# Performance work log

Measured on AMD Instinct MI355X. Metric: run time of the kernel, lower is better.

Reference implementation:

```python
import jax, jax.numpy as jnp
import numpy as np

G, T, S, M = 2048, 256, 32, 8


def setup_inputs() -> dict:
    key = jax.random.key(0)
    k_in, k_F, k_H, k_Q, k_R = jax.random.split(key, 5)
    inp = jax.random.normal(k_in, (G, T, M), dtype=jnp.float32)
    I_s = jnp.eye(S, dtype=jnp.float32)
    # Stable transition matrix: near-identity with small random perturbation
    F = 0.95 * I_s + 0.05 * jax.random.normal(k_F, (S, S), dtype=jnp.float32) / jnp.sqrt(S * 1.0)
    H = jax.random.normal(k_H, (M, S), dtype=jnp.float32) / jnp.sqrt(S * 1.0)
    Lq = jax.random.normal(k_Q, (S, S), dtype=jnp.float32) / jnp.sqrt(S * 1.0)
    Q = 0.01 * (Lq @ Lq.T) + 1e-4 * I_s  # process noise (PSD)
    Lr = jax.random.normal(k_R, (M, M), dtype=jnp.float32) / jnp.sqrt(M * 1.0)
    R = 0.1 * (Lr @ Lr.T) + 1e-3 * jnp.eye(M, dtype=jnp.float32)  # measurement noise (PSD)
    m0 = jnp.zeros((G, S), dtype=jnp.float32)
    P0 = jnp.broadcast_to(I_s, (G, S, S)).astype(jnp.float32)
    return {"input": inp, "F": F, "H": H, "Q": Q, "R": R, "m0": m0, "P0": P0}


def _kalman_filter(inp, F, H, Q, R, m0, P0):
    """One-step-ahead measurement predictions, matching KalmanFilter.forward:
    at each t emit measurement of the prior, then update with obs[t] and predict."""

    def step(carry, obs_t):
        m, P = carry  # m: [G,S], P: [G,S,S] (prior at time t)
        # --- compute_measurement(H, R) on the prior ---
        meas_mean = m @ H.T                                   # [G,M]
        HP = jnp.einsum('ms,gsk->gmk', H, P)                  # [G,M,S]
        S_t = jnp.einsum('gmk,nk->gmn', HP, H) + R            # [G,M,M]
        # --- update(obs_t) ---
        resid = obs_t - meas_mean                             # [G,M]
        KT = jnp.linalg.solve(S_t, HP)                        # [G,M,S] = S^{-1} H P = K^T
        m_upd = m + jnp.einsum('gms,gm->gs', KT, resid)       # [G,S]
        P_upd = P - jnp.einsum('gmi,gmk->gik', KT, HP)        # (I-KH)P
        P_upd = 0.5 * (P_upd + jnp.swapaxes(P_upd, -1, -2))   # symmetrize (numerics)
        # --- predict(F, Q) ---
        m_next = m_upd @ F.T
        P_next = jnp.einsum('ij,gjk,lk->gil', F, P_upd, F) + Q
        return (m_next, P_next), (meas_mean, S_t)

    obs_T = jnp.swapaxes(inp, 0, 1)                           # [T,G,M]
    _, (means, covs) = jax.lax.scan(step, (m0, P0), obs_T)
    return jnp.swapaxes(means, 0, 1), jnp.swapaxes(covs, 0, 1)  # [G,T,M], [G,T,M,M]


def reference(input, F, H, Q, R, m0, P0):
    return _kalman_filter(input, F, H, Q, R, m0, P0)
```

## Files before the change

kernel.cpp:

```cpp
#include <hip/hip_runtime.h>

#define G_N 2048
#define T_N 256
#define S_N 32
#define M_N 8

#define A_OFF 0
#define B_OFF 262144
#define S_OFF (262144 + 65536)

#define OUT_TOTAL 37748736ull
#define EL 3072
#define SCRATCH_FLOATS (EL + 2ull * 256 * EL)

__global__ __launch_bounds__(1024) void kf_init(
    const float* __restrict__ F, const float* __restrict__ H,
    const float* __restrict__ Q, const float* __restrict__ R,
    float* __restrict__ base)
{
    __shared__ float Hs[8][33], Rl[8][9], Rinv[8][9], RH[8][33];
    const int tid = threadIdx.x;
    if (tid < 256) Hs[tid >> 5][tid & 31] = H[tid];
    if (tid < 64)  Rl[tid >> 3][tid & 7] = R[tid];
    __syncthreads();
    if (tid < 64) {
        int r = tid >> 3, c = tid & 7;
        float a = Rl[r][c];
        float b = (r == c) ? 1.f : 0.f;
#pragma unroll
        for (int j = 0; j < 8; ++j) {
            float ajj  = __shfl(a, j * 8 + j, 64);
            float pinv = 1.0f / ajj;
            if (r == j) { a *= pinv; b *= pinv; }
            float ajc = __shfl(a, j * 8 + c, 64);
            float bjc = __shfl(b, j * 8 + c, 64);
            float arj = __shfl(a, r * 8 + j, 64);
            if (r != j) { a -= arj * ajc; b -= arj * bjc; }
        }
        Rinv[r][c] = b;
    }
    __syncthreads();
    if (tid < 256) {
        int m = tid >> 5, j = tid & 31;
        float s = 0.f;
#pragma unroll
        for (int n = 0; n < 8; ++n) s += Rinv[m][n] * Hs[n][j];
        RH[m][j] = s;
    }
    __syncthreads();
    {
        int i = tid >> 5, j = tid & 31;
        float g = 0.f;
#pragma unroll
        for (int m = 0; m < 8; ++m) g += Hs[m][i] * RH[m][j];
        base[2048 + tid] = g;
    }
    base[tid] = Q[tid];
    base[1024 + tid] = F[tid];
}

__global__ __launch_bounds__(1024) void kf_level(
    const float* __restrict__ in, float* __restrict__ out,
    const float* __restrict__ base, int dist)
{
    const int bi = blockIdx.x;
    const int tid = threadIdx.x;
    const int r = tid >> 5, c = tid & 31;
    float* o = out + (size_t)bi * EL;

    if (bi < dist) {
        const float* s = base ? base : in + (size_t)bi * EL;
        o[tid] = s[tid]; o[tid + 1024] = s[tid + 1024]; o[tid + 2048] = s[tid + 2048];
        return;
    }
    const float* pa = base ? base : in + (size_t)(bi - dist) * EL;
    const float* pb = base ? base : in + (size_t)bi * EL;

    __shared__ float Ea[32][33], Fa[32][33], Ga[32][33];
    __shared__ float Eb[32][33], Fb[32][33], Gb[32][33];
    __shared__ float T1[32][33], T3[32][33], T4[32][33], T5[32][33], T6[32][33];
    __shared__ float Kf[32][33], Msv[32][33];
    __shared__ float Aug[32][67];

    Ea[r][c] = pa[tid]; Fa[r][c] = pa[tid + 1024]; Ga[r][c] = pa[tid + 2048];
    Eb[r][c] = pb[tid]; Fb[r][c] = pb[tid + 1024]; Gb[r][c] = pb[tid + 2048];
    __syncthreads();

    {
        float acc = (r == c) ? 1.f : 0.f;
#pragma unroll
        for (int k = 0; k < 32; ++k) acc += Gb[r][k] * Ea[k][c];
        Aug[r][c] = acc; Msv[r][c] = acc;
        Aug[r][32 + c] = (r == c) ? 1.f : 0.f;
    }
    __syncthreads();

    for (int jb = 0; jb < 16; ++jb) {
        const int p0 = 2 * jb, p1 = p0 + 1;
        float a00 = Aug[p0][p0], a01 = Aug[p0][p1], a10 = Aug[p1][p0], a11 = Aug[p1][p1];
        float m0 = Aug[r][p0], m1 = Aug[r][p1];
        float q0 = Aug[p0][c], q1 = Aug[p1][c];
        float q0b = Aug[p0][32 + c], q1b = Aug[p1][32 + c];
        float x0 = Aug[r][c], x1 = Aug[r][32 + c];
        __syncthreads();
        float id = 1.0f / (a00 * a11 - a01 * a10);
        float i00 = a11 * id, i01 = -a01 * id, i10 = -a10 * id, i11 = a00 * id;
        float n0, n1;
        if (r == p0)      { n0 = i00 * q0 + i01 * q1;  n1 = i00 * q0b + i01 * q1b; }
        else if (r == p1) { n0 = i10 * q0 + i11 * q1;  n1 = i10 * q0b + i11 * q1b; }
        else {
            float L0 = m0 * i00 + m1 * i10, L1 = m0 * i01 + m1 * i11;
            n0 = x0 - L0 * q0 - L1 * q1;
            n1 = x1 - L0 * q0b - L1 * q1b;
        }
        Aug[r][c] = n0; Aug[r][32 + c] = n1;
        __syncthreads();
    }

    {
        float acc = 0.f;
#pragma unroll
        for (int k = 0; k < 32; ++k) acc += Msv[r][k] * Aug[k][32 + c];
        T6[r][c] = acc;
    }
    __syncthreads();
    {
        float acc = 0.f;
#pragma unroll
        for (int k = 0; k < 32; ++k) acc += Aug[r][32 + k] * T6[k][c];
        Kf[r][c] = 2.0f * Aug[r][32 + c] - acc;
    }
    __syncthreads();

    {
        float a1 = 0.f, a3 = 0.f, a4 = 0.f;
#pragma unroll
        for (int k = 0; k < 32; ++k) {
            a1 += Ea[r][k] * Kf[k][c];
            a3 += Fb[r][k] * Kf[c][k];
            a4 += Kf[r][k] * Gb[k][c];
        }
        T1[r][c] = a1; T3[r][c] = a3; T4[r][c] = a4;
    }
    __syncthreads();
    {
        float b1 = 0.f, b2 = 0.f;
#pragma unroll
        for (int k = 0; k < 32; ++k) {
            b1 += Fb[r][k] * T1[k][c];
            b2 += T3[r][k] * Fa[k][c];
        }
        T6[r][c] = b1; T5[r][c] = b2;
    }
    __syncthreads();
    {
        float c1 = Eb[r][c], c2 = 0.f;
#pragma unroll
        for (int k = 0; k < 32; ++k) {
            c1 += T6[r][k] * Fb[c][k];
            c2 += Fa[k][r] * T4[k][c];
        }
        Msv[r][c] = c1; T1[r][c] = c2;
    }
    __syncthreads();
    {
        float d1 = Ga[r][c];
#pragma unroll
        for (int k = 0; k < 32; ++k) d1 += T1[r][k] * Fa[k][c];
        T3[r][c] = d1;
    }
    __syncthreads();
    o[tid]        = 0.5f * (Msv[r][c] + Msv[c][r]);
    o[1024 + tid] = T5[r][c];
    o[2048 + tid] = 0.5f * (T3[r][c] + T3[c][r]);
}

__global__ __launch_bounds__(1024) void kf_final(
    const float* __restrict__ elems, const float* __restrict__ F,
    const float* __restrict__ H, const float* __restrict__ R,
    const float* __restrict__ P0, float* __restrict__ ws)
{
    const int t = blockIdx.x;
    const int tid = threadIdx.x;
    const int r = tid >> 5, c = tid & 31;

    __shared__ float Pm[32][33], Fs[32][33], P0s[32][33];
    __shared__ float Et[32][33], Ft[32][33], Gt[32][33], Yv[32][33], Tt[32][33];
    __shared__ float Hs[8][33], HP[8][33], Wm[8][33], Um[8][33];
    __shared__ float Ss[8][9], Rs[8][9], Si[8][9];
    __shared__ float Aug[32][67];

    Fs[r][c] = F[tid];
    if (tid < 256) Hs[tid >> 5][tid & 31] = H[tid];
    if (tid < 64)  Rs[tid >> 3][tid & 7] = R[tid];
    P0s[r][c] = P0[tid];
    __syncthreads();

    if (t == 0) {
        Pm[r][c] = P0s[r][c];
        __syncthreads();
    } else {
        const float* el = elems + (size_t)(t - 1) * EL;
        Et[r][c] = el[tid]; Ft[r][c] = el[tid + 1024]; Gt[r][c] = el[tid + 2048];
        __syncthreads();
        {
            float acc = (r == c) ? 1.f : 0.f;
#pragma unroll
            for (int k = 0; k < 32; ++k) acc += Gt[r][k] * P0s[k][c];
            Aug[r][c] = acc;
            Aug[r][32 + c] = (r == c) ? 1.f : 0.f;
        }
        __syncthreads();
        for (int jb = 0; jb < 16; ++jb) {
            const int p0 = 2 * jb, p1 = p0 + 1;
            float a00 = Aug[p0][p0], a01 = Aug[p0][p1], a10 = Aug[p1][p0], a11 = Aug[p1][p1];
            float m0 = Aug[r][p0], m1 = Aug[r][p1];
            float q0 = Aug[p0][c], q1 = Aug[p1][c];
            float q0b = Aug[p0][32 + c], q1b = Aug[p1][32 + c];
            float x0 = Aug[r][c], x1 = Aug[r][32 + c];
            __syncthreads();
            float id = 1.0f / (a00 * a11 - a01 * a10);
            float i00 = a11 * id, i01 = -a01 * id, i10 = -a10 * id, i11 = a00 * id;
            float n0, n1;
            if (r == p0)      { n0 = i00 * q0 + i01 * q1;  n1 = i00 * q0b + i01 * q1b; }
            else if (r == p1) { n0 = i10 * q0 + i11 * q1;  n1 = i10 * q0b + i11 * q1b; }
            else {
                float L0 = m0 * i00 + m1 * i10, L1 = m0 * i01 + m1 * i11;
                n0 = x0 - L0 * q0 - L1 * q1;
                n1 = x1 - L0 * q0b - L1 * q1b;
            }
            Aug[r][c] = n0; Aug[r][32 + c] = n1;
            __syncthreads();
        }
        {
            float acc = 0.f;
#pragma unroll
            for (int k = 0; k < 32; ++k) acc += P0s[r][k] * Aug[k][32 + c];
            Yv[r][c] = acc;
        }
        __syncthreads();
        {
            float acc = 0.f;
#pragma unroll
            for (int k = 0; k < 32; ++k) acc += Ft[r][k] * Yv[k][c];
            Tt[r][c] = acc;
        }
        __syncthreads();
        {
            float acc = Et[r][c];
#pragma unroll
            for (int k = 0; k < 32; ++k) acc += Tt[r][k] * Ft[c][k];
            Pm[r][c] = acc;
        }
        __syncthreads();
        {
            float ps = 0.5f * (Pm[r][c] + Pm[c][r]);
            __syncthreads();
            Pm[r][c] = ps;
            __syncthreads();
        }
    }

    float* A_tab = ws + A_OFF;
    float* B_tab = ws + B_OFF;
    float* S_tab = ws + S_OFF;

    if (tid < 256) {
        int m = tid >> 5, k = tid & 31;
        float acc = 0.f;
#pragma unroll
        for (int j = 0; j < 32; ++j) acc += Hs[m][j] * Pm[j][k];
        HP[m][k] = acc;
    }
    __syncthreads();
    if (tid < 64) {
        int m = tid >> 3, n = tid & 7;
        float sv = Rs[m][n];
#pragma unroll
        for (int k = 0; k < 32; ++k) sv += HP[m][k] * Hs[n][k];
        Ss[m][n] = sv;
        S_tab[t * 64 + m * 8 + n] = sv;
    }
    if (tid >= 256 && tid < 512) {
        int e = tid - 256, m = e >> 5, j = e & 31;
        float wv = 0.f;
#pragma unroll
        for (int k = 0; k < 32; ++k) wv += HP[m][k] * Fs[j][k];
        Wm[m][j] = wv;
    }
    __syncthreads();
    if (tid < 64) {
        int rr = tid >> 3, cc = tid & 7;
        float a = Ss[rr][cc];
        float b = (rr == cc) ? 1.f : 0.f;
#pragma unroll
        for (int j = 0; j < 8; ++j) {
            float ajj  = __shfl(a, j * 8 + j, 64);
            float pinv = 1.0f / ajj;
            if (rr == j) { a *= pinv; b *= pinv; }
            float ajc = __shfl(a, j * 8 + cc, 64);
            float bjc = __shfl(b, j * 8 + cc, 64);
            float arj = __shfl(a, rr * 8 + j, 64);
            if (rr != j) { a -= arj * ajc; b -= arj * bjc; }
        }
        Si[rr][cc] = b;
    }
    __syncthreads();
    if (tid < 256) {
        int m = tid >> 5, s = tid & 31;
        float u = 0.f;
#pragma unroll
        for (int n = 0; n < 8; ++n) u += Si[m][n] * Wm[n][s];
        Um[m][s] = u;
        B_tab[t * 256 + s * 8 + m] = u;
    }
    __syncthreads();
    {
        float a = Fs[r][c];
#pragma unroll
        for (int m = 0; m < 8; ++m) a -= Um[m][r] * Hs[m][c];
        A_tab[t * 1024 + tid] = a;
    }
}

__global__ __launch_bounds__(256) void kf_means(
    const float* __restrict__ obs, const float* __restrict__ H,
    const float* __restrict__ m0, const float* __restrict__ ws,
    float* __restrict__ out)
{
    __shared__ float As[S_N][36];
    __shared__ float Bs[S_N][12];
    __shared__ float4 Sls[16];

    const int tid = threadIdx.x;
    const int gl = tid >> 5, s = tid & 31;
    const int g = blockIdx.x * 8 + gl;

    const float4* A4 = (const float4*)(ws + A_OFF);
    const float4* B4 = (const float4*)(ws + B_OFF);
    const float4* S4 = (const float4*)(ws + S_OFF);
    float* means = out;
    float4* covs4 = (float4*)(out + (size_t)G_N * T_N * M_N);

    float Hreg[32];
#pragma unroll
    for (int k = 0; k < 32; ++k) Hreg[k] = (s < 8) ? H[s * 32 + k] : 0.f;

    float m_reg = m0[blockIdx.x * 256 + tid];

    float4 a4p = A4[tid];
    float4 b4p = (tid < 64) ? B4[tid] : make_float4(0, 0, 0, 0);
    float4 s4p = (tid < 16) ? S4[tid] : make_float4(0, 0, 0, 0);
    float u_reg = (s < 8) ? obs[((size_t)g * T_N + 0) * M_N + s] : 0.f;

    for (int t = 0; t < T_N; ++t) {
        {
            int rr = tid >> 3, c4w = tid & 7;
            *(float4*)&As[rr][4 * (((2 * rr) ^ c4w) & 7)] = a4p;
        }
        if (tid < 64) *(float4*)&Bs[tid >> 1][4 * (tid & 1)] = b4p;
        if (tid < 16) Sls[tid] = s4p;
        __syncthreads();

        if (t + 1 < T_N) {
            a4p = A4[(t + 1) * 256 + tid];
            if (tid < 64) b4p = B4[(t + 1) * 64 + tid];
            if (tid < 16) s4p = S4[(t + 1) * 16 + tid];
        }
        float u_next = 0.f;
        if (t + 1 < T_N && s < 8) u_next = obs[((size_t)g * T_N + (t + 1)) * M_N + s];

        if (tid < 128) {
            int gl2 = tid >> 4, cc = tid & 15;
            covs4[((size_t)(blockIdx.x * 8 + gl2) * T_N + t) * 16 + cc] = Sls[cc];
        }

        float acc = 0.f, accH = 0.f;
#pragma unroll
        for (int c4 = 0; c4 < 8; ++c4) {
            float4 a = *(const float4*)&As[s][4 * (((2 * s) ^ c4) & 7)];
            float mk0 = __shfl(m_reg, 4 * c4 + 0, 32);
            float mk1 = __shfl(m_reg, 4 * c4 + 1, 32);
            float mk2 = __shfl(m_reg, 4 * c4 + 2, 32);
            float mk3 = __shfl(m_reg, 4 * c4 + 3, 32);
            acc  += a.x * mk0 + a.y * mk1 + a.z * mk2 + a.w * mk3;
            accH += Hreg[4 * c4 + 0] * mk0 + Hreg[4 * c4 + 1] * mk1
                  + Hreg[4 * c4 + 2] * mk2 + Hreg[4 * c4 + 3] * mk3;
        }
#pragma unroll
        for (int mm = 0; mm < 8; ++mm) acc += Bs[s][mm] * __shfl(u_reg, mm, 32);

        if (s < 8) means[((size_t)g * T_N + t) * M_N + s] = accH;
        m_reg = acc;
        u_reg = u_next;
        __syncthreads();
    }
}

extern "C" void kernel_launch(void* const* d_in, const int* in_sizes, int n_in,
                              void* d_out, int out_size, void* d_ws, size_t ws_size,
                              hipStream_t stream) {
    const float* obs = (const float*)d_in[0];
    const float* F   = (const float*)d_in[1];
    const float* H   = (const float*)d_in[2];
    const float* Q   = (const float*)d_in[3];
    const float* R   = (const float*)d_in[4];
    const float* m0  = (const float*)d_in[5];
    const float* P0  = (const float*)d_in[6];
    float* out = (float*)d_out;
    float* ws  = (float*)d_ws;

    float* scratch = out + (OUT_TOTAL - SCRATCH_FLOATS);
    float* base = scratch;
    float* bufA = scratch + EL;
    float* bufB = bufA + 256ull * EL;

    kf_init<<<1, 1024, 0, stream>>>(F, H, Q, R, base);
    kf_level<<<256, 1024, 0, stream>>>(nullptr, bufA, base, 1);
    kf_level<<<256, 1024, 0, stream>>>(bufA, bufB, nullptr, 2);
    kf_level<<<256, 1024, 0, stream>>>(bufB, bufA, nullptr, 4);
    kf_level<<<256, 1024, 0, stream>>>(bufA, bufB, nullptr, 8);
    kf_level<<<256, 1024, 0, stream>>>(bufB, bufA, nullptr, 16);
    kf_level<<<256, 1024, 0, stream>>>(bufA, bufB, nullptr, 32);
    kf_level<<<256, 1024, 0, stream>>>(bufB, bufA, nullptr, 64);
    kf_level<<<256, 1024, 0, stream>>>(bufA, bufB, nullptr, 128);
    kf_final<<<256, 1024, 0, stream>>>(bufB, F, H, R, P0, ws);
    kf_means<<<G_N / 8, 256, 0, stream>>>(obs, H, m0, ws, out);
}
```

Measured before the change: 435.3 us.

## Replace prefix-scan levels with power-of-two compositions and chunked mean recurrence

The eight-level parallel prefix scan over covariance elements is replaced by a single-block computation of power-of-two compositions. A 31-block kernel then builds the composites, and each time step needs at most one extra composition. The sequential mean recurrence is split into 16 time chunks run in parallel with zero start state, then corrected by propagating chunk-end states through precomputed transition products and H-projected tables. This is meant to cut the launch count and serial depth, and to spread the mean work across more blocks. In exchange it adds scratch traffic in the output buffer and a separate cleanup pass for the tail covariance writes.

```diff
diff --git a/kernel.cpp b/kernel.cpp
--- a/kernel.cpp
+++ b/kernel.cpp
@@ -2,99 +2,45 @@
 
 #define G_N 2048
 #define T_N 256
-#define S_N 32
-#define M_N 8
 
 #define A_OFF 0
 #define B_OFF 262144
-#define S_OFF (262144 + 65536)
-
-#define OUT_TOTAL 37748736ull
-#define EL 3072
-#define SCRATCH_FLOATS (EL + 2ull * 256 * EL)
-
-__global__ __launch_bounds__(1024) void kf_init(
-    const float* __restrict__ F, const float* __restrict__ H,
-    const float* __restrict__ Q, const float* __restrict__ R,
-    float* __restrict__ base)
-{
-    __shared__ float Hs[8][33], Rl[8][9], Rinv[8][9], RH[8][33];
-    const int tid = threadIdx.x;
-    if (tid < 256) Hs[tid >> 5][tid & 31] = H[tid];
-    if (tid < 64)  Rl[tid >> 3][tid & 7] = R[tid];
-    __syncthreads();
+#define S_OFF 327680
+
+#define OUT_TOTAL  37748736ull
+#define EL         3072
+#define MEND_OFF   36498432ull
+#define HT_OFF     37547008ull
+#define PHI_OFF    37612544ull
+#define PW2_OFF    37628928ull
+#define PHP_OFF    37644288ull
+#define XT_OFF     37653504ull
+#define YT_OFF     37702656ull
+#define COVS4_BASE 1048576ull
+#define TAIL4_SKIP 8076032ull
+
+__device__ __forceinline__ void inv8_wave(int tid, float (*A8)[9], float (*O8)[9]) {
     if (tid < 64) {
         int r = tid >> 3, c = tid & 7;
-        float a = Rl[r][c];
+        float a = A8[r][c];
         float b = (r == c) ? 1.f : 0.f;
 #pragma unroll
         for (int j = 0; j < 8; ++j) {
-            float ajj  = __shfl(a, j * 8 + j, 64);
-            float pinv = 1.0f / ajj;
-            if (r == j) { a *= pinv; b *= pinv; }
+            float ajj = __shfl(a, j * 8 + j, 64);
+            float pv = 1.0f / ajj;
+            if (r == j) { a *= pv; b *= pv; }
             float ajc = __shfl(a, j * 8 + c, 64);
             float bjc = __shfl(b, j * 8 + c, 64);
             float arj = __shfl(a, r * 8 + j, 64);
             if (r != j) { a -= arj * ajc; b -= arj * bjc; }
         }
-        Rinv[r][c] = b;
-    }
-    __syncthreads();
-    if (tid < 256) {
-        int m = tid >> 5, j = tid & 31;
-        float s = 0.f;
-#pragma unroll
-        for (int n = 0; n < 8; ++n) s += Rinv[m][n] * Hs[n][j];
-        RH[m][j] = s;
-    }
-    __syncthreads();
-    {
-        int i = tid >> 5, j = tid & 31;
-        float g = 0.f;
-#pragma unroll
-        for (int m = 0; m < 8; ++m) g += Hs[m][i] * RH[m][j];
-        base[2048 + tid] = g;
-    }
-    base[tid] = Q[tid];
-    base[1024 + tid] = F[tid];
-}
-
-__global__ __launch_bounds__(1024) void kf_level(
-    const float* __restrict__ in, float* __restrict__ out,
-    const float* __restrict__ base, int dist)
-{
-    const int bi = blockIdx.x;
-    const int tid = threadIdx.x;
+        O8[r][c] = b;
+    }
+}
+
+__device__ __forceinline__ void inv32(int tid, float (*Aug)[66],
+                                      float (*Msv)[33], float (*Tmp)[33]) {
     const int r = tid >> 5, c = tid & 31;
-    float* o = out + (size_t)bi * EL;
-
-    if (bi < dist) {
-        const float* s = base ? base : in + (size_t)bi * EL;
-        o[tid] = s[tid]; o[tid + 1024] = s[tid + 1024]; o[tid + 2048] = s[tid + 2048];
-        return;
-    }
-    const float* pa = base ? base : in + (size_t)(bi - dist) * EL;
-    const float* pb = base ? base : in + (size_t)bi * EL;
-
-    __shared__ float Ea[32][33], Fa[32][33], Ga[32][33];
-    __shared__ float Eb[32][33], Fb[32][33], Gb[32][33];
-    __shared__ float T1[32][33], T3[32][33], T4[32][33], T5[32][33], T6[32][33];
-    __shared__ float Kf[32][33], Msv[32][33];
-    __shared__ float Aug[32][67];
-
-    Ea[r][c] = pa[tid]; Fa[r][c] = pa[tid + 1024]; Ga[r][c] = pa[tid + 2048];
-    Eb[r][c] = pb[tid]; Fb[r][c] = pb[tid + 1024]; Gb[r][c] = pb[tid + 2048];
-    __syncthreads();
-
-    {
-        float acc = (r == c) ? 1.f : 0.f;
-#pragma unroll
-        for (int k = 0; k < 32; ++k) acc += Gb[r][k] * Ea[k][c];
-        Aug[r][c] = acc; Msv[r][c] = acc;
-        Aug[r][32 + c] = (r == c) ? 1.f : 0.f;
-    }
-    __syncthreads();
-
     for (int jb = 0; jb < 16; ++jb) {
         const int p0 = 2 * jb, p1 = p0 + 1;
         float a00 = Aug[p0][p0], a01 = Aug[p0][p1], a10 = Aug[p1][p0], a11 = Aug[p1][p1];
@@ -116,161 +62,225 @@
         Aug[r][c] = n0; Aug[r][32 + c] = n1;
         __syncthreads();
     }
-
+    float acc = 0.f;
+#pragma unroll
+    for (int k = 0; k < 32; ++k) acc += Msv[r][k] * Aug[k][32 + c];
+    Tmp[r][c] = acc;
+    __syncthreads();
+    acc = 0.f;
+#pragma unroll
+    for (int k = 0; k < 32; ++k) acc += Aug[r][32 + k] * Tmp[k][c];
+    float kv = 2.0f * Aug[r][32 + c] - acc;
+    __syncthreads();
+    Aug[r][c] = kv;
+    __syncthreads();
+}
+
+__device__ __forceinline__ void compose(int tid,
+    float (*Ea)[33], float (*Fa)[33], float (*Ga)[33],
+    float (*Eb)[33], float (*Fb)[33], float (*Gb)[33],
+    float (*Msv)[33], float (*T1)[33], float (*T3)[33],
+    float (*T4)[33], float (*T5)[33], float (*Aug)[66]) {
+    const int r = tid >> 5, c = tid & 31;
+    float acc = (r == c) ? 1.f : 0.f;
+#pragma unroll
+    for (int k = 0; k < 32; ++k) acc += Gb[r][k] * Ea[k][c];
+    Aug[r][c] = acc; Msv[r][c] = acc; Aug[r][32 + c] = (r == c) ? 1.f : 0.f;
+    __syncthreads();
+    inv32(tid, Aug, Msv, T4);
+    float a1 = 0, a3 = 0, a4 = 0;
+#pragma unroll
+    for (int k = 0; k < 32; ++k) {
+        a1 += Ea[r][k] * Aug[k][c];
+        a3 += Fb[r][k] * Aug[c][k];
+        a4 += Aug[r][k] * Gb[k][c];
+    }
+    T1[r][c] = a1; T3[r][c] = a3; T4[r][c] = a4;
+    __syncthreads();
+    float b1 = 0, b2 = 0;
+#pragma unroll
+    for (int k = 0; k < 32; ++k) {
+        b1 += Fb[r][k] * T1[k][c];
+        b2 += T3[r][k] * Fa[k][c];
+    }
+    Aug[r][32 + c] = b1; T5[r][c] = b2;
+    __syncthreads();
+    float c1 = Eb[r][c], c2 = 0;
+#pragma unroll
+    for (int k = 0; k < 32; ++k) {
+        c1 += Aug[r][32 + k] * Fb[c][k];
+        c2 += Fa[k][r] * T4[k][c];
+    }
+    __syncthreads();
+    Msv[r][c] = c1; T1[r][c] = c2;
+    __syncthreads();
+    float d1 = Ga[r][c];
+#pragma unroll
+    for (int k = 0; k < 32; ++k) d1 += T1[r][k] * Fa[k][c];
+    __syncthreads();
+    T3[r][c] = d1;
+    __syncthreads();
+}
+
+__device__ __forceinline__ void load_el(const float* g, int tid,
+    float (*E)[33], float (*F)[33], float (*G)[33]) {
+    const int r = tid >> 5, c = tid & 31;
+    E[r][c] = g[tid]; F[r][c] = g[tid + 1024]; G[r][c] = g[tid + 2048];
+}
+__device__ __forceinline__ void store_el(float* g, int tid,
+    float (*E)[33], float (*F)[33], float (*G)[33]) {
+    const int r = tid >> 5, c = tid & 31;
+    g[tid] = E[r][c]; g[tid + 1024] = F[r][c]; g[tid + 2048] = G[r][c];
+}
+__device__ __forceinline__ void copy_res_sym(int tid,
+    float (*Msv)[33], float (*T5)[33], float (*T3)[33],
+    float (*E)[33], float (*F)[33], float (*G)[33]) {
+    const int r = tid >> 5, c = tid & 31;
+    float e = 0.5f * (Msv[r][c] + Msv[c][r]);
+    float f = T5[r][c];
+    float gg = 0.5f * (T3[r][c] + T3[c][r]);
+    E[r][c] = e; F[r][c] = f; G[r][c] = gg;
+    __syncthreads();
+}
+
+#define COMPOSE_SHARED \
+    __shared__ float Ea[32][33], Fa[32][33], Ga[32][33]; \
+    __shared__ float Eb[32][33], Fb[32][33], Gb[32][33]; \
+    __shared__ float Msv[32][33], T1[32][33], T3[32][33], T4[32][33], T5[32][33]; \
+    __shared__ float Aug[32][66];
+
+__global__ __launch_bounds__(1024) void kf_pow1(
+    const float* __restrict__ F, const float* __restrict__ H,
+    const float* __restrict__ Q, const float* __restrict__ R,
+    float* __restrict__ out)
+{
+    COMPOSE_SHARED
+    __shared__ float Rl[8][9], Ri[8][9];
+    const int tid = threadIdx.x, r = tid >> 5, c = tid & 31;
+
+    Ea[r][c] = Q[tid];
+    Fa[r][c] = F[tid];
+    if (tid < 256) T1[tid >> 5][tid & 31] = H[tid];
+    if (tid < 64)  Rl[tid >> 3][tid & 7] = R[tid];
+    __syncthreads();
+    inv8_wave(tid, Rl, Ri);
+    __syncthreads();
+    if (tid < 256) {
+        int m = tid >> 5, j = tid & 31;
+        float s = 0.f;
+#pragma unroll
+        for (int n = 0; n < 8; ++n) s += Ri[m][n] * T1[n][j];
+        T3[m][j] = s;
+    }
+    __syncthreads();
     {
-        float acc = 0.f;
-#pragma unroll
-        for (int k = 0; k < 32; ++k) acc += Msv[r][k] * Aug[k][32 + c];
-        T6[r][c] = acc;
-    }
-    __syncthreads();
-    {
-        float acc = 0.f;
-#pragma unroll
-        for (int k = 0; k < 32; ++k) acc += Aug[r][32 + k] * T6[k][c];
-        Kf[r][c] = 2.0f * Aug[r][32 + c] - acc;
-    }
-    __syncthreads();
-
-    {
-        float a1 = 0.f, a3 = 0.f, a4 = 0.f;
-#pragma unroll
-        for (int k = 0; k < 32; ++k) {
-            a1 += Ea[r][k] * Kf[k][c];
-            a3 += Fb[r][k] * Kf[c][k];
-            a4 += Kf[r][k] * Gb[k][c];
-        }
-        T1[r][c] = a1; T3[r][c] = a3; T4[r][c] = a4;
-    }
-    __syncthreads();
-    {
-        float b1 = 0.f, b2 = 0.f;
-#pragma unroll
-        for (int k = 0; k < 32; ++k) {
-            b1 += Fb[r][k] * T1[k][c];
-            b2 += T3[r][k] * Fa[k][c];
-        }
-        T6[r][c] = b1; T5[r][c] = b2;
-    }
-    __syncthreads();
-    {
-        float c1 = Eb[r][c], c2 = 0.f;
-#pragma unroll
-        for (int k = 0; k < 32; ++k) {
-            c1 += T6[r][k] * Fb[c][k];
-            c2 += Fa[k][r] * T4[k][c];
-        }
-        Msv[r][c] = c1; T1[r][c] = c2;
-    }
-    __syncthreads();
-    {
-        float d1 = Ga[r][c];
-#pragma unroll
-        for (int k = 0; k < 32; ++k) d1 += T1[r][k] * Fa[k][c];
-        T3[r][c] = d1;
-    }
-    __syncthreads();
-    o[tid]        = 0.5f * (Msv[r][c] + Msv[c][r]);
-    o[1024 + tid] = T5[r][c];
-    o[2048 + tid] = 0.5f * (T3[r][c] + T3[c][r]);
+        float g2 = 0.f;
+#pragma unroll
+        for (int m = 0; m < 8; ++m) g2 += T1[m][r] * T3[m][c];
+        Ga[r][c] = g2;
+    }
+    __syncthreads();
+
+    float* PW2 = out + PW2_OFF;
+    store_el(PW2, tid, Ea, Fa, Ga);
+    for (int k = 1; k <= 4; ++k) {
+        compose(tid, Ea, Fa, Ga, Ea, Fa, Ga, Msv, T1, T3, T4, T5, Aug);
+        copy_res_sym(tid, Msv, T5, T3, Ea, Fa, Ga);
+        store_el(PW2 + (size_t)k * EL, tid, Ea, Fa, Ga);
+    }
+    float* PHP = out + PHP_OFF;
+    for (int j = 1; j <= 3; ++j) {
+        compose(tid, Ea, Fa, Ga, Ea, Fa, Ga, Msv, T1, T3, T4, T5, Aug);
+        copy_res_sym(tid, Msv, T5, T3, Ea, Fa, Ga);
+        store_el(PHP + (size_t)(j - 1) * EL, tid, Ea, Fa, Ga);
+    }
+}
+
+__global__ __launch_bounds__(1024) void kf_pow2(float* __restrict__ out)
+{
+    COMPOSE_SHARED
+    const int tid = threadIdx.x, b = blockIdx.x;
+    const int isY = (b >= 16);
+    const int val = isY ? (b - 15) : (b + 1);
+    const float* tb = out + PW2_OFF + (isY ? 4 * (size_t)EL : 0);
+    float* dst = isY ? (out + YT_OFF + (size_t)(b - 16) * EL)
+                     : (out + XT_OFF + (size_t)b * EL);
+
+    int bits[5], nb = 0;
+    for (int j = 0; j < 5; ++j) if ((val >> j) & 1) bits[nb++] = j;
+
+    load_el(tb + (size_t)bits[0] * EL, tid, Ea, Fa, Ga);
+    __syncthreads();
+    for (int bi = 1; bi < nb; ++bi) {
+        load_el(tb + (size_t)bits[bi] * EL, tid, Eb, Fb, Gb);
+        __syncthreads();
+        compose(tid, Ea, Fa, Ga, Eb, Fb, Gb, Msv, T1, T3, T4, T5, Aug);
+        copy_res_sym(tid, Msv, T5, T3, Ea, Fa, Ga);
+    }
+    store_el(dst, tid, Ea, Fa, Ga);
 }
 
 __global__ __launch_bounds__(1024) void kf_final(
-    const float* __restrict__ elems, const float* __restrict__ F,
-    const float* __restrict__ H, const float* __restrict__ R,
-    const float* __restrict__ P0, float* __restrict__ ws)
-{
-    const int t = blockIdx.x;
-    const int tid = threadIdx.x;
-    const int r = tid >> 5, c = tid & 31;
-
-    __shared__ float Pm[32][33], Fs[32][33], P0s[32][33];
-    __shared__ float Et[32][33], Ft[32][33], Gt[32][33], Yv[32][33], Tt[32][33];
+    const float* __restrict__ Fg, const float* __restrict__ Hg,
+    const float* __restrict__ Rg, const float* __restrict__ P0,
+    const float* __restrict__ outc, float* __restrict__ ws)
+{
+    COMPOSE_SHARED
     __shared__ float Hs[8][33], HP[8][33], Wm[8][33], Um[8][33];
     __shared__ float Ss[8][9], Rs[8][9], Si[8][9];
-    __shared__ float Aug[32][67];
-
-    Fs[r][c] = F[tid];
-    if (tid < 256) Hs[tid >> 5][tid & 31] = H[tid];
-    if (tid < 64)  Rs[tid >> 3][tid & 7] = R[tid];
-    P0s[r][c] = P0[tid];
-    __syncthreads();
+    const int t = blockIdx.x, tid = threadIdx.x, r = tid >> 5, c = tid & 31;
 
     if (t == 0) {
-        Pm[r][c] = P0s[r][c];
+        Eb[r][c] = P0[tid];
         __syncthreads();
     } else {
-        const float* el = elems + (size_t)(t - 1) * EL;
-        Et[r][c] = el[tid]; Ft[r][c] = el[tid + 1024]; Gt[r][c] = el[tid + 2048];
-        __syncthreads();
-        {
-            float acc = (r == c) ? 1.f : 0.f;
-#pragma unroll
-            for (int k = 0; k < 32; ++k) acc += Gt[r][k] * P0s[k][c];
-            Aug[r][c] = acc;
-            Aug[r][32 + c] = (r == c) ? 1.f : 0.f;
-        }
-        __syncthreads();
-        for (int jb = 0; jb < 16; ++jb) {
-            const int p0 = 2 * jb, p1 = p0 + 1;
-            float a00 = Aug[p0][p0], a01 = Aug[p0][p1], a10 = Aug[p1][p0], a11 = Aug[p1][p1];
-            float m0 = Aug[r][p0], m1 = Aug[r][p1];
-            float q0 = Aug[p0][c], q1 = Aug[p1][c];
-            float q0b = Aug[p0][32 + c], q1b = Aug[p1][32 + c];
-            float x0 = Aug[r][c], x1 = Aug[r][32 + c];
+        const int i = t - 1, s = (i & 15) + 1, q = i >> 4;
+        if (q == 0) {
+            load_el(outc + XT_OFF + (size_t)(s - 1) * EL, tid, Msv, T5, T3);
             __syncthreads();
-            float id = 1.0f / (a00 * a11 - a01 * a10);
-            float i00 = a11 * id, i01 = -a01 * id, i10 = -a10 * id, i11 = a00 * id;
-            float n0, n1;
-            if (r == p0)      { n0 = i00 * q0 + i01 * q1;  n1 = i00 * q0b + i01 * q1b; }
-            else if (r == p1) { n0 = i10 * q0 + i11 * q1;  n1 = i10 * q0b + i11 * q1b; }
-            else {
-                float L0 = m0 * i00 + m1 * i10, L1 = m0 * i01 + m1 * i11;
-                n0 = x0 - L0 * q0 - L1 * q1;
-                n1 = x1 - L0 * q0b - L1 * q1b;
-            }
-            Aug[r][c] = n0; Aug[r][32 + c] = n1;
+        } else {
+            load_el(outc + XT_OFF + (size_t)(s - 1) * EL, tid, Ea, Fa, Ga);
+            load_el(outc + YT_OFF + (size_t)(q - 1) * EL, tid, Eb, Fb, Gb);
             __syncthreads();
-        }
-        {
-            float acc = 0.f;
-#pragma unroll
-            for (int k = 0; k < 32; ++k) acc += P0s[r][k] * Aug[k][32 + c];
-            Yv[r][c] = acc;
-        }
-        __syncthreads();
-        {
-            float acc = 0.f;
-#pragma unroll
-            for (int k = 0; k < 32; ++k) acc += Ft[r][k] * Yv[k][c];
-            Tt[r][c] = acc;
-        }
-        __syncthreads();
-        {
-            float acc = Et[r][c];
-#pragma unroll
-            for (int k = 0; k < 32; ++k) acc += Tt[r][k] * Ft[c][k];
-            Pm[r][c] = acc;
-        }
-        __syncthreads();
-        {
-            float ps = 0.5f * (Pm[r][c] + Pm[c][r]);
-            __syncthreads();
-            Pm[r][c] = ps;
-            __syncthreads();
-        }
-    }
-
-    float* A_tab = ws + A_OFF;
-    float* B_tab = ws + B_OFF;
-    float* S_tab = ws + S_OFF;
-
+            compose(tid, Ea, Fa, Ga, Eb, Fb, Gb, Msv, T1, T3, T4, T5, Aug);
+        }
+        Ea[r][c] = P0[tid];
+        __syncthreads();
+        float acc = (r == c) ? 1.f : 0.f;
+#pragma unroll
+        for (int k = 0; k < 32; ++k) acc += T3[r][k] * Ea[k][c];
+        Aug[r][c] = acc; T1[r][c] = acc; Aug[r][32 + c] = (r == c) ? 1.f : 0.f;
+        __syncthreads();
+        inv32(tid, Aug, T1, T4);
+        acc = 0.f;
+#pragma unroll
+        for (int k = 0; k < 32; ++k) acc += Ea[r][k] * Aug[k][c];
+        T4[r][c] = acc;
+        __syncthreads();
+        acc = 0.f;
+#pragma unroll
+        for (int k = 0; k < 32; ++k) acc += T5[r][k] * T4[k][c];
+        Fa[r][c] = acc;
+        __syncthreads();
+        acc = Msv[r][c];
+#pragma unroll
+        for (int k = 0; k < 32; ++k) acc += Fa[r][k] * T5[c][k];
+        Ga[r][c] = acc;
+        __syncthreads();
+        Eb[r][c] = 0.5f * (Ga[r][c] + Ga[c][r]);
+        __syncthreads();
+    }
+
+    T1[r][c] = Fg[tid];
+    if (tid < 256) Hs[tid >> 5][tid & 31] = Hg[tid];
+    if (tid < 64)  Rs[tid >> 3][tid & 7] = Rg[tid];
+    __syncthreads();
     if (tid < 256) {
-        int m = tid >> 5, k = tid & 31;
-        float acc = 0.f;
-#pragma unroll
-        for (int j = 0; j < 32; ++j) acc += Hs[m][j] * Pm[j][k];
-        HP[m][k] = acc;
+        int m = tid >> 5, k2 = tid & 31;
+        float a = 0.f;
+#pragma unroll
+        for (int j = 0; j < 32; ++j) a += Hs[m][j] * Eb[j][k2];
+        HP[m][k2] = a;
     }
     __syncthreads();
     if (tid < 64) {
@@ -279,101 +289,109 @@
 #pragma unroll
         for (int k = 0; k < 32; ++k) sv += HP[m][k] * Hs[n][k];
         Ss[m][n] = sv;
-        S_tab[t * 64 + m * 8 + n] = sv;
+        ws[S_OFF + (size_t)t * 64 + tid] = sv;
     }
     if (tid >= 256 && tid < 512) {
         int e = tid - 256, m = e >> 5, j = e & 31;
         float wv = 0.f;
 #pragma unroll
-        for (int k = 0; k < 32; ++k) wv += HP[m][k] * Fs[j][k];
+        for (int k = 0; k < 32; ++k) wv += HP[m][k] * T1[j][k];
         Wm[m][j] = wv;
     }
     __syncthreads();
-    if (tid < 64) {
-        int rr = tid >> 3, cc = tid & 7;
-        float a = Ss[rr][cc];
-        float b = (rr == cc) ? 1.f : 0.f;
-#pragma unroll
-        for (int j = 0; j < 8; ++j) {
-            float ajj  = __shfl(a, j * 8 + j, 64);
-            float pinv = 1.0f / ajj;
-            if (rr == j) { a *= pinv; b *= pinv; }
-            float ajc = __shfl(a, j * 8 + cc, 64);
-            float bjc = __shfl(b, j * 8 + cc, 64);
-            float arj = __shfl(a, rr * 8 + j, 64);
-            if (rr != j) { a -= arj * ajc; b -= arj * bjc; }
-        }
-        Si[rr][cc] = b;
-    }
+    inv8_wave(tid, Ss, Si);
     __syncthreads();
     if (tid < 256) {
-        int m = tid >> 5, s = tid & 31;
+        int m = tid >> 5, s2 = tid & 31;
         float u = 0.f;
 #pragma unroll
-        for (int n = 0; n < 8; ++n) u += Si[m][n] * Wm[n][s];
-        Um[m][s] = u;
-        B_tab[t * 256 + s * 8 + m] = u;
+        for (int n = 0; n < 8; ++n) u += Si[m][n] * Wm[n][s2];
+        Um[m][s2] = u;
+        ws[B_OFF + (size_t)t * 256 + s2 * 8 + m] = u;
     }
     __syncthreads();
     {
-        float a = Fs[r][c];
+        float a = T1[r][c];
 #pragma unroll
         for (int m = 0; m < 8; ++m) a -= Um[m][r] * Hs[m][c];
-        A_tab[t * 1024 + tid] = a;
-    }
-}
-
-__global__ __launch_bounds__(256) void kf_means(
-    const float* __restrict__ obs, const float* __restrict__ H,
-    const float* __restrict__ m0, const float* __restrict__ ws,
+        ws[A_OFF + (size_t)t * 1024 + tid] = a;
+    }
+}
+
+__global__ __launch_bounds__(1024) void kf_tpre(
+    const float* __restrict__ Hg, const float* __restrict__ ws,
     float* __restrict__ out)
 {
-    __shared__ float As[S_N][36];
-    __shared__ float Bs[S_N][12];
-    __shared__ float4 Sls[16];
-
-    const int tid = threadIdx.x;
-    const int gl = tid >> 5, s = tid & 31;
-    const int g = blockIdx.x * 8 + gl;
-
+    __shared__ float Ta[32][33], Tb[32][33], As[32][33], Hs[8][33];
+    const int cc = blockIdx.x, tid = threadIdx.x, r = tid >> 5, j = tid & 31;
+    const int t0 = 16 * cc;
+    float* HT = out + HT_OFF;
+    float* PHI = out + PHI_OFF;
+    const float* A_tab = ws + A_OFF;
+
+    Ta[r][j] = (r == j) ? 1.f : 0.f;
+    if (tid < 256) { Hs[tid >> 5][tid & 31] = Hg[tid]; HT[(size_t)t0 * 256 + tid] = Hg[tid]; }
+    __syncthreads();
+
+    float (*cur)[33] = Ta, (*nxt)[33] = Tb;
+    for (int k = 1; k <= 16; ++k) {
+        As[r][j] = A_tab[(size_t)(t0 + k - 1) * 1024 + tid];
+        __syncthreads();
+        float a = 0.f;
+#pragma unroll
+        for (int q = 0; q < 32; ++q) a += As[r][q] * cur[q][j];
+        nxt[r][j] = a;
+        __syncthreads();
+        { float (*tmp)[33] = cur; cur = nxt; nxt = tmp; }
+        if (k < 16) {
+            if (tid < 256) {
+                int m = tid >> 5, s2 = tid & 31;
+                float h = 0.f;
+#pragma unroll
+                for (int j2 = 0; j2 < 32; ++j2) h += Hs[m][j2] * cur[j2][s2];
+                HT[(size_t)(t0 + k) * 256 + tid] = h;
+            }
+        } else {
+            PHI[(size_t)cc * 1024 + tid] = cur[r][j];
+        }
+    }
+}
+
+__global__ __launch_bounds__(256) void kf_m1(
+    const float* __restrict__ obs, const float* __restrict__ Hg,
+    const float* __restrict__ ws, float* __restrict__ out)
+{
+    __shared__ float As[32][36];
+    __shared__ float Bs[32][12];
+    const int tid = threadIdx.x, gl = tid >> 5, s = tid & 31;
+    const int cc = blockIdx.x >> 8;
+    const int gg = blockIdx.x & 255;
+    const size_t g = (size_t)gg * 8 + gl;
+    const int t0 = 16 * cc;
     const float4* A4 = (const float4*)(ws + A_OFF);
     const float4* B4 = (const float4*)(ws + B_OFF);
-    const float4* S4 = (const float4*)(ws + S_OFF);
     float* means = out;
-    float4* covs4 = (float4*)(out + (size_t)G_N * T_N * M_N);
+    float* MEND = out + MEND_OFF;
 
     float Hreg[32];
 #pragma unroll
-    for (int k = 0; k < 32; ++k) Hreg[k] = (s < 8) ? H[s * 32 + k] : 0.f;
-
-    float m_reg = m0[blockIdx.x * 256 + tid];
-
-    float4 a4p = A4[tid];
-    float4 b4p = (tid < 64) ? B4[tid] : make_float4(0, 0, 0, 0);
-    float4 s4p = (tid < 16) ? S4[tid] : make_float4(0, 0, 0, 0);
-    float u_reg = (s < 8) ? obs[((size_t)g * T_N + 0) * M_N + s] : 0.f;
-
-    for (int t = 0; t < T_N; ++t) {
-        {
-            int rr = tid >> 3, c4w = tid & 7;
-            *(float4*)&As[rr][4 * (((2 * rr) ^ c4w) & 7)] = a4p;
-        }
+    for (int k = 0; k < 32; ++k) Hreg[k] = (s < 8) ? Hg[s * 32 + k] : 0.f;
+
+    float m_reg = 0.f;
+    float4 a4p = A4[(size_t)t0 * 256 + tid];
+    float4 b4p = (tid < 64) ? B4[(size_t)t0 * 64 + tid] : make_float4(0, 0, 0, 0);
+    float u_reg = (s < 8) ? obs[(g * 256 + t0) * 8 + s] : 0.f;
+
+    for (int k = 0; k < 16; ++k) {
+        const int t = t0 + k;
+        { int rr = tid >> 3, c4w = tid & 7; *(float4*)&As[rr][4 * (((2 * rr) ^ c4w) & 7)] = a4p; }
         if (tid < 64) *(float4*)&Bs[tid >> 1][4 * (tid & 1)] = b4p;
-        if (tid < 16) Sls[tid] = s4p;
-        __syncthreads();
-
-        if (t + 1 < T_N) {
-            a4p = A4[(t + 1) * 256 + tid];
-            if (tid < 64) b4p = B4[(t + 1) * 64 + tid];
-            if (tid < 16) s4p = S4[(t + 1) * 16 + tid];
-        }
-        float u_next = 0.f;
-        if (t + 1 < T_N && s < 8) u_next = obs[((size_t)g * T_N + (t + 1)) * M_N + s];
-
-        if (tid < 128) {
-            int gl2 = tid >> 4, cc = tid & 15;
-            covs4[((size_t)(blockIdx.x * 8 + gl2) * T_N + t) * 16 + cc] = Sls[cc];
-        }
+        __syncthreads();
+        if (k < 15) {
+            a4p = A4[(size_t)(t + 1) * 256 + tid];
+            if (tid < 64) b4p = B4[(size_t)(t + 1) * 64 + tid];
+        }
+        float u_next = (k < 15 && s < 8) ? obs[(g * 256 + t + 1) * 8 + s] : 0.f;
 
         float acc = 0.f, accH = 0.f;
 #pragma unroll
@@ -384,16 +402,87 @@
             float mk2 = __shfl(m_reg, 4 * c4 + 2, 32);
             float mk3 = __shfl(m_reg, 4 * c4 + 3, 32);
             acc  += a.x * mk0 + a.y * mk1 + a.z * mk2 + a.w * mk3;
-            accH += Hreg[4 * c4 + 0] * mk0 + Hreg[4 * c4 + 1] * mk1
+            accH += Hreg[4 * c4] * mk0 + Hreg[4 * c4 + 1] * mk1
                   + Hreg[4 * c4 + 2] * mk2 + Hreg[4 * c4 + 3] * mk3;
         }
 #pragma unroll
         for (int mm = 0; mm < 8; ++mm) acc += Bs[s][mm] * __shfl(u_reg, mm, 32);
 
-        if (s < 8) means[((size_t)g * T_N + t) * M_N + s] = accH;
-        m_reg = acc;
-        u_reg = u_next;
-        __syncthreads();
+        if (s < 8) means[(g * 256 + t) * 8 + s] = accH;
+        m_reg = acc; u_reg = u_next;
+        __syncthreads();
+    }
+    MEND[(g * 16 + cc) * 32 + s] = m_reg;
+}
+
+__global__ __launch_bounds__(256) void kf_m23(
+    const float* __restrict__ m0, const float* __restrict__ ws,
+    float* __restrict__ out)
+{
+    __shared__ float mst[8][16][32];
+    const int tid = threadIdx.x, gl = tid >> 5, s = tid & 31;
+    const size_t g = (size_t)blockIdx.x * 8 + gl;
+    const float* MEND = out + MEND_OFF;
+    const float* HT = out + HT_OFF;
+    const float* PHI = out + PHI_OFF;
+    float* means = out;
+    float4* out4 = (float4*)out;
+    const float4* S4 = (const float4*)(ws + S_OFF);
+
+    float msr = m0[g * 32 + s];
+    for (int cc = 0; cc < 16; ++cc) {
+        mst[gl][cc][s] = msr;
+        if (cc < 15) {
+            const float4* ph = (const float4*)(PHI + (size_t)cc * 1024 + s * 32);
+            float nv = MEND[(g * 16 + cc) * 32 + s];
+#pragma unroll
+            for (int q4 = 0; q4 < 8; ++q4) {
+                float4 p = ph[q4];
+                nv += p.x * __shfl(msr, 4 * q4 + 0, 32) + p.y * __shfl(msr, 4 * q4 + 1, 32)
+                    + p.z * __shfl(msr, 4 * q4 + 2, 32) + p.w * __shfl(msr, 4 * q4 + 3, 32);
+            }
+            msr = nv;
+        }
+    }
+    __syncthreads();
+
+    const int m = s & 7, tq = s >> 3;
+    for (int cc = 0; cc < 16; ++cc) {
+#pragma unroll
+        for (int it = 0; it < 4; ++it) {
+            int t = cc * 16 + it * 4 + tq;
+            const float4* hr = (const float4*)(HT + (size_t)t * 256 + m * 32);
+            float corr = 0.f;
+#pragma unroll
+            for (int q4 = 0; q4 < 8; ++q4) {
+                float4 h = hr[q4];
+                corr += h.x * mst[gl][cc][4 * q4] + h.y * mst[gl][cc][4 * q4 + 1]
+                      + h.z * mst[gl][cc][4 * q4 + 2] + h.w * mst[gl][cc][4 * q4 + 3];
+            }
+            means[g * 2048 + (size_t)t * 8 + m] += corr;
+        }
+    }
+    for (int tp = 0; tp < 128; ++tp) {
+        int t = 2 * tp + (s >> 4);
+        int e4 = s & 15;
+        size_t rel4 = (g * 256 + t) * 16 + e4;
+        if (rel4 < TAIL4_SKIP) out4[COVS4_BASE + rel4] = S4[t * 16 + e4];
+    }
+}
+
+__global__ void kf_clean(const float* __restrict__ ws, float* __restrict__ out)
+{
+    float4* out4 = (float4*)out;
+    const float4* S4 = (const float4*)(ws + S_OFF);
+    const size_t start = COVS4_BASE + TAIL4_SKIP;
+    const size_t end = OUT_TOTAL / 4;
+    size_t i = start + (size_t)blockIdx.x * blockDim.x + threadIdx.x;
+    const size_t stride = (size_t)gridDim.x * blockDim.x;
+    for (; i < end; i += stride) {
+        size_t rel = i - COVS4_BASE;
+        int t = (int)((rel >> 4) & 255);
+        int e4 = (int)(rel & 15);
+        out4[i] = S4[t * 16 + e4];
     }
 }
 
@@ -410,20 +499,11 @@
     float* out = (float*)d_out;
     float* ws  = (float*)d_ws;
 
-    float* scratch = out + (OUT_TOTAL - SCRATCH_FLOATS);
-    float* base = scratch;
-    float* bufA = scratch + EL;
-    float* bufB = bufA + 256ull * EL;
-
-    kf_init<<<1, 1024, 0, stream>>>(F, H, Q, R, base);
-    kf_level<<<256, 1024, 0, stream>>>(nullptr, bufA, base, 1);
-    kf_level<<<256, 1024, 0, stream>>>(bufA, bufB, nullptr, 2);
-    kf_level<<<256, 1024, 0, stream>>>(bufB, bufA, nullptr, 4);
-    kf_level<<<256, 1024, 0, stream>>>(bufA, bufB, nullptr, 8);
-    kf_level<<<256, 1024, 0, stream>>>(bufB, bufA, nullptr, 16);
-    kf_level<<<256, 1024, 0, stream>>>(bufA, bufB, nullptr, 32);
-    kf_level<<<256, 1024, 0, stream>>>(bufB, bufA, nullptr, 64);
-    kf_level<<<256, 1024, 0, stream>>>(bufA, bufB, nullptr, 128);
-    kf_final<<<256, 1024, 0, stream>>>(bufB, F, H, R, P0, ws);
-    kf_means<<<G_N / 8, 256, 0, stream>>>(obs, H, m0, ws, out);
-}
+    kf_pow1 <<<1,    1024, 0, stream>>>(F, H, Q, R, out);
+    kf_pow2 <<<31,   1024, 0, stream>>>(out);
+    kf_final<<<256,  1024, 0, stream>>>(F, H, R, P0, out, ws);
+    kf_tpre <<<16,   1024, 0, stream>>>(H, ws, out);
+    kf_m1   <<<4096, 256,  0, stream>>>(obs, H, ws, out);
+    kf_m23  <<<256,  256,  0, stream>>>(m0, ws, out);
+    kf_clean<<<512,  256,  0, stream>>>(ws, out);
+}
```

New measurement: 590.5 us. 1.36x slower.
